# Kernel tuning notes

Hardware: AMD Instinct MI355X
Metric: run time of the kernel (lower is better)

Reference implementation:

```python
import jax, jax.numpy as jnp
import numpy as np


def setup_inputs() -> dict:
    key = jax.random.key(0)
    ks = jax.random.split(key, 6)
    B, T, D, H = 2, 2048, 1024, 16
    dk = D // H
    s = 0.02
    return {
        "x": jax.random.normal(ks[0], (B, T, D), dtype=jnp.float32),
        "Wq": jax.random.normal(ks[1], (H, dk, dk), dtype=jnp.float32) * s,
        "Wk": jax.random.normal(ks[2], (H, dk, dk), dtype=jnp.float32) * s,
        "Wv": jax.random.normal(ks[3], (H, dk, dk), dtype=jnp.float32) * s,
        "Wp": jax.random.normal(ks[4], (D, D), dtype=jnp.float32) * s,
        "bp": jnp.zeros((D,), dtype=jnp.float32),
    }


def reference(x, Wq, Wk, Wv, Wp, bp):
    B, T, D = x.shape
    H, dk, _ = Wq.shape
    # split into heads: [B, H, T, dk]
    xh = x.reshape(B, T, H, dk).transpose(0, 2, 1, 3)
    # per-head torch Linear (y = x @ W^T), all heads at once
    q = jnp.einsum('bhtd,hkd->bhtk', xh, Wq)
    k = jnp.einsum('bhtd,hkd->bhtk', xh, Wk)
    v = jnp.einsum('bhtd,hkd->bhtk', xh, Wv)
    scale = 1.0 / jnp.sqrt(jnp.float32(dk))  # original divides by sqrt(C) with C == d_k
    scores = jnp.einsum('bhqd,bhkd->bhqk', q, k) * scale
    causal = jnp.tril(jnp.ones((T, T), dtype=bool))
    scores = jnp.where(causal[None, None], scores, -jnp.inf)
    attn = jax.nn.softmax(scores, axis=-1)
    out = jnp.einsum('bhqk,bhkd->bhqd', attn, v)  # [B,H,T,dk]
    out = out.transpose(0, 2, 1, 3).reshape(B, T, D)  # concat heads
    return out @ Wp.T + bp
```

## Files before the change

### kernel.cpp

```cpp
#include <hip/hip_runtime.h>
#include <math.h>

#define B_ 2
#define T_ 2048
#define D_ 1024
#define H_ 16
#define DK 64
#define BH_ (B_*H_)

typedef __attribute__((ext_vector_type(8))) short short8;
typedef __attribute__((ext_vector_type(4))) short bf16x4;
typedef __attribute__((ext_vector_type(4))) float fragC;

__device__ __forceinline__ unsigned short f2bf(float x) {
    union { float f; unsigned u; } c; c.f = x;
    unsigned r = c.u + 0x7fff + ((c.u >> 16) & 1);
    return (unsigned short)(r >> 16);
}

__device__ __forceinline__ unsigned short f2bf_trunc(float x) {
    union { float f; unsigned u; } c; c.f = x;
    return (unsigned short)(c.u >> 16);
}

__device__ __forceinline__ unsigned pack2bf(float a, float b) {
    return (unsigned)f2bf(a) | ((unsigned)f2bf(b) << 16);
}

__device__ __forceinline__ short8 packbf8(float4 a, float4 b) {
    union { short8 v; unsigned u[4]; } r;
    r.u[0] = pack2bf(a.x, a.y); r.u[1] = pack2bf(a.z, a.w);
    r.u[2] = pack2bf(b.x, b.y); r.u[3] = pack2bf(b.z, b.w);
    return r.v;
}

__device__ __forceinline__ int swz(int row, int unit) {
    return row*64 + (((unit ^ (row & 7)) << 3));
}

__device__ __forceinline__ void gload_lds16(const void* g, void* l) {
    __builtin_amdgcn_global_load_lds(
        (const __attribute__((address_space(1))) unsigned int*)g,
        (__attribute__((address_space(3))) unsigned int*)l, 16, 0, 0);
}

__global__ __launch_bounds__(256) void cvt_kernel(
    const float* __restrict__ Wp,
    const float* __restrict__ Wq, const float* __restrict__ Wk,
    const float* __restrict__ Wv,
    unsigned short* __restrict__ Wb, unsigned short* __restrict__ wqkvb)
{
    const int gid = blockIdx.x * 256 + threadIdx.x;
    const float* src; unsigned short* dst;
    if (gid < 131072) { src = Wp + (size_t)gid * 8; dst = Wb + (size_t)gid * 8; }
    else              { int e = gid - 131072;
                        int mat = e >> 13, rem = e & 8191;
                        int h = rem >> 9, od = rem & 511;
                        const float* ws = (mat == 0) ? Wq : (mat == 1) ? Wk : Wv;
                        src = ws + ((size_t)(h << 9) + od) * 8;
                        dst = wqkvb + ((size_t)h*1536 + mat*512 + od) * 8; }
    float4 a = *(const float4*)src;
    float4 b = *(const float4*)(src + 4);
    *(uint4*)dst = make_uint4(pack2bf(a.x, a.y), pack2bf(a.z, a.w),
                              pack2bf(b.x, b.y), pack2bf(b.z, b.w));
}

__global__ __launch_bounds__(256) void qkv_kernel(
    const float* __restrict__ x,
    const unsigned short* __restrict__ wqkvb,
    unsigned short* __restrict__ q, unsigned short* __restrict__ k,
    unsigned short* __restrict__ vt)
{
    __shared__ unsigned short Wl[3*64*64];

    const int bh = blockIdx.x;
    const int b  = bh >> 4, h = bh & 15;
    const int t0 = blockIdx.y * 128;
    const int tid = threadIdx.x;
    const int wave = tid >> 6, lane = tid & 63;
    const int n = lane & 15, quad = lane >> 4;

    {
        const unsigned short* wsrc = wqkvb + (size_t)h * 12288;
        #pragma unroll
        for (int j = 0; j < 6; ++j) {
            const int off = (wave*6 + j) * 512 + lane*8;
            gload_lds16(wsrc + off, &Wl[off]);
        }
    }

    const int tw = t0 + wave*32;
    short8 xf[2][2];
    #pragma unroll
    for (int rt = 0; rt < 2; ++rt) {
        const float* xr = &x[((size_t)b*T_ + tw + rt*16 + n)*D_ + h*DK];
        float4 a0 = *(const float4*)&xr[quad*8];
        float4 a1 = *(const float4*)&xr[quad*8 + 4];
        xf[rt][0] = packbf8(a0, a1);
        float4 b0 = *(const float4*)&xr[32 + quad*8];
        float4 b1 = *(const float4*)&xr[32 + quad*8 + 4];
        xf[rt][1] = packbf8(b0, b1);
    }
    __syncthreads();

    const int tb0 = blockIdx.y*8 + wave*2;
    #pragma unroll
    for (int mat = 0; mat < 3; ++mat) {
        const int wbase = mat * 4096;
        #pragma unroll
        for (int ct = 0; ct < 4; ++ct) {
            short8 wf0 = *(const short8*)&Wl[wbase + (ct*16 + n)*64 + quad*8];
            short8 wf1 = *(const short8*)&Wl[wbase + (ct*16 + n)*64 + 32 + quad*8];
            #pragma unroll
            for (int rt = 0; rt < 2; ++rt) {
                fragC z = {0.f,0.f,0.f,0.f};
                if (mat < 2) {
                    z = __builtin_amdgcn_mfma_f32_16x16x32_bf16(wf0, xf[rt][0], z, 0,0,0);
                    z = __builtin_amdgcn_mfma_f32_16x16x32_bf16(wf1, xf[rt][1], z, 0,0,0);
                    unsigned short* dstg = (mat == 0) ? q : k;
                    unsigned short* dp = &dstg[((size_t)bh*128 + tb0 + rt)*1024
                                               + (ct*2 + (quad>>1))*128 + n*8 + (quad&1)*4];
                    *(uint2*)dp = make_uint2(pack2bf(z[0], z[1]), pack2bf(z[2], z[3]));
                } else {
                    z = __builtin_amdgcn_mfma_f32_16x16x32_bf16(xf[rt][0], wf0, z, 0,0,0);
                    z = __builtin_amdgcn_mfma_f32_16x16x32_bf16(xf[rt][1], wf1, z, 0,0,0);
                    unsigned short* dp = &vt[((size_t)bh*DK + ct*16 + n)*T_
                                             + tw + rt*16 + quad*4];
                    *(uint2*)dp = make_uint2(pack2bf(z[0], z[1]), pack2bf(z[2], z[3]));
                }
            }
        }
    }
}

__global__ __launch_bounds__(256, 4) void attn_kernel(
    const unsigned short* __restrict__ q, const unsigned short* __restrict__ k,
    const unsigned short* __restrict__ vt, unsigned short* __restrict__ aout)
{
    __shared__ unsigned short Ks[64*64];
    __shared__ unsigned short Vs[64*64];
    __shared__ unsigned short Ps[4][16][68];

    const int id = blockIdx.x;
    int qt, bh;
    if (id < 512) { bh = id >> 4;         qt = 31 - (id & 15); }
    else          { bh = (id - 512) >> 4; qt = (id - 512) & 15; }

    const int b   = bh >> 4, h = bh & 15;
    const int tid = threadIdx.x;
    const int wave = tid >> 6, lane = tid & 63;
    const int n = lane & 15, quad = lane >> 4;

    const int q0 = qt*64 + wave*16;

    const unsigned short* qb = &q[((size_t)bh*128 + qt*4 + wave)*1024 + n*8];
    short8 qf0 = *(const short8*)&qb[quad*128];
    short8 qf1 = *(const short8*)&qb[(4 + quad)*128];

    fragC o[4];
    #pragma unroll
    for (int dt = 0; dt < 4; ++dt) o[dt] = (fragC){0.f,0.f,0.f,0.f};
    fragC l4 = {0.f,0.f,0.f,0.f};

    short8 ones;
    #pragma unroll
    for (int j = 0; j < 8; ++j) ones[j] = (short)0x3F80;

    const int srow = tid >> 2;
    const int u0   = (tid & 3) * 2;
    const unsigned short* kg = &k[(size_t)bh*131072
                                  + (srow >> 4)*1024 + u0*128 + (srow & 15)*8];
    const unsigned short* vg = &vt[((size_t)bh*DK + srow)*T_ + u0*8];
    const int kl0 = swz(srow, u0), kl1 = swz(srow, u0+1);

    const int nt = qt + 1;
    short8 pk0 = *(const short8*)&kg[0], pk1 = *(const short8*)&kg[128];
    short8 pv0 = *(const short8*)&vg[0], pv1 = *(const short8*)&vg[8];

    const float sc = 0.125f * 1.44269504088896340736f;

    for (int kt = 0; kt < nt; ++kt) {
        __syncthreads();
        *(short8*)&Ks[kl0] = pk0; *(short8*)&Ks[kl1] = pk1;
        *(short8*)&Vs[kl0] = pv0; *(short8*)&Vs[kl1] = pv1;
        __syncthreads();
        if (kt + 1 < nt) {
            pk0 = *(const short8*)&kg[(size_t)(kt+1)*4096];
            pk1 = *(const short8*)&kg[(size_t)(kt+1)*4096 + 128];
            pv0 = *(const short8*)&vg[(kt+1)*64];
            pv1 = *(const short8*)&vg[(kt+1)*64 + 8];
        }
        const bool diag = (kt == qt);

        #pragma unroll
        for (int ct = 0; ct < 4; ++ct) {
            const int row = ct*16 + n;
            short8 kf0 = *(const short8*)&Ks[swz(row, quad)];
            short8 kf1 = *(const short8*)&Ks[swz(row, 4 + quad)];
            fragC c = {0.f,0.f,0.f,0.f};
            c = __builtin_amdgcn_mfma_f32_16x16x32_bf16(kf0, qf0, c, 0,0,0);
            c = __builtin_amdgcn_mfma_f32_16x16x32_bf16(kf1, qf1, c, 0,0,0);
            float p[4];
            #pragma unroll
            for (int r = 0; r < 4; ++r) p[r] = exp2f(c[r] * sc);
            if (diag) {
                const int lim = (wave*16 + n) - (ct*16 + quad*4);
                #pragma unroll
                for (int r = 0; r < 4; ++r) if (r > lim) p[r] = 0.f;
            }
            union { uint2 u; unsigned short s[4]; } w;
            w.s[0] = f2bf_trunc(p[0]); w.s[1] = f2bf_trunc(p[1]);
            w.s[2] = f2bf_trunc(p[2]); w.s[3] = f2bf_trunc(p[3]);
            *(uint2*)&Ps[wave][n][ct*16 + quad*4] = w.u;
        }
        bf16x4 a0 = *(const bf16x4*)&Ps[wave][n][quad*8];
        bf16x4 a1 = *(const bf16x4*)&Ps[wave][n][quad*8 + 4];
        bf16x4 a2 = *(const bf16x4*)&Ps[wave][n][32 + quad*8];
        bf16x4 a3 = *(const bf16x4*)&Ps[wave][n][32 + quad*8 + 4];
        short8 pf0 = __builtin_shufflevector(a0, a1, 0,1,2,3,4,5,6,7);
        short8 pf1 = __builtin_shufflevector(a2, a3, 0,1,2,3,4,5,6,7);
        l4 = __builtin_amdgcn_mfma_f32_16x16x32_bf16(ones, pf0, l4, 0,0,0);
        l4 = __builtin_amdgcn_mfma_f32_16x16x32_bf16(ones, pf1, l4, 0,0,0);
        #pragma unroll
        for (int dt = 0; dt < 4; ++dt) {
            const int row = dt*16 + n;
            short8 vf0 = *(const short8*)&Vs[swz(row, quad)];
            short8 vf1 = *(const short8*)&Vs[swz(row, 4 + quad)];
            o[dt] = __builtin_amdgcn_mfma_f32_16x16x32_bf16(vf0, pf0, o[dt], 0,0,0);
            o[dt] = __builtin_amdgcn_mfma_f32_16x16x32_bf16(vf1, pf1, o[dt], 0,0,0);
        }
    }

    const float inv = 1.0f / l4[0];
    unsigned short* dp = &aout[((size_t)b*T_ + q0 + n)*D_ + h*DK + quad*4];
    #pragma unroll
    for (int dt = 0; dt < 4; ++dt) {
        *(uint2*)(dp + dt*16) =
            make_uint2(pack2bf(o[dt][0]*inv, o[dt][1]*inv),
                       pack2bf(o[dt][2]*inv, o[dt][3]*inv));
    }
}

__global__ __launch_bounds__(256) void proj_kernel(
    const unsigned short* __restrict__ A, const unsigned short* __restrict__ Wb,
    const float* __restrict__ bp, float* __restrict__ out)
{
    __shared__ unsigned short As[128*64];
    __shared__ unsigned short Bs[128*64];

    const int m0 = blockIdx.x * 128, n0 = blockIdx.y * 128;
    const int tid = threadIdx.x;
    const int wave = tid >> 6, lane = tid & 63;
    const int wm = wave & 1, wn = wave >> 1;
    const int n = lane & 15, quad = lane >> 4;

    const int srow = wave*32 + (lane >> 3);
    const int scol = (lane & 7) * 8;
    const unsigned short* ag = &A [(size_t)(m0 + srow)*1024 + scol];
    const unsigned short* bg = &Wb[(size_t)(n0 + srow)*1024 + scol];
    unsigned short* al = &As[(size_t)srow*64 + scol];
    unsigned short* bl = &Bs[(size_t)srow*64 + scol];

    fragC acc[4][4];
    #pragma unroll
    for (int i = 0; i < 4; ++i)
        #pragma unroll
        for (int j = 0; j < 4; ++j) acc[i][j] = (fragC){0.f,0.f,0.f,0.f};

    for (int kt = 0; kt < 16; ++kt) {
        __syncthreads();
        #pragma unroll
        for (int i = 0; i < 4; ++i) {
            gload_lds16(ag + (size_t)i*8*1024 + kt*64, al + i*8*64);
            gload_lds16(bg + (size_t)i*8*1024 + kt*64, bl + i*8*64);
        }
        __syncthreads();

        #pragma unroll
        for (int kk = 0; kk < 2; ++kk) {
            short8 af[4], bf[4];
            #pragma unroll
            for (int i = 0; i < 4; ++i)
                af[i] = *(const short8*)&As[(wm*64 + i*16 + n)*64 + kk*32 + quad*8];
            #pragma unroll
            for (int j = 0; j < 4; ++j)
                bf[j] = *(const short8*)&Bs[(wn*64 + j*16 + n)*64 + kk*32 + quad*8];
            #pragma unroll
            for (int i = 0; i < 4; ++i)
                #pragma unroll
                for (int j = 0; j < 4; ++j)
                    acc[i][j] = __builtin_amdgcn_mfma_f32_16x16x32_bf16(af[i], bf[j], acc[i][j], 0,0,0);
        }
    }

    #pragma unroll
    for (int i = 0; i < 4; ++i) {
        #pragma unroll
        for (int r = 0; r < 4; ++r) {
            const int m = m0 + wm*64 + i*16 + quad*4 + r;
            #pragma unroll
            for (int j = 0; j < 4; ++j) {
                const int col = n0 + wn*64 + j*16 + n;
                out[(size_t)m*1024 + col] = acc[i][j][r] + bp[col];
            }
        }
    }
}

extern "C" void kernel_launch(void* const* d_in, const int* in_sizes, int n_in,
                              void* d_out, int out_size, void* d_ws, size_t ws_size,
                              hipStream_t stream)
{
    const float* x  = (const float*)d_in[0];
    const float* Wq = (const float*)d_in[1];
    const float* Wk = (const float*)d_in[2];
    const float* Wv = (const float*)d_in[3];
    const float* Wp = (const float*)d_in[4];
    const float* bp = (const float*)d_in[5];
    float* out = (float*)d_out;

    const size_t per = (size_t)BH_ * T_ * DK;
    unsigned short* qws   = (unsigned short*)d_ws;
    unsigned short* kws   = qws + per;
    unsigned short* vtws  = kws + per;
    unsigned short* aws   = vtws + per;
    unsigned short* wbws  = aws + per;
    unsigned short* wqkvb = wbws + 1024*1024;

    cvt_kernel<<<dim3(608), 256, 0, stream>>>(Wp, Wq, Wk, Wv, wbws, wqkvb);
    qkv_kernel<<<dim3(BH_, T_/128), 256, 0, stream>>>(x, wqkvb, qws, kws, vtws);
    attn_kernel<<<dim3(1024), 256, 0, stream>>>(qws, kws, vtws, aws);
    proj_kernel<<<dim3(32, 8), 256, 0, stream>>>(aws, wbws, bp, out);
}
```

Baseline: 153.6 us.

## Keep P in registers and double-buffer K/V via direct LDS loads

The QKV kernel now folds the softmax scale into Q and writes V in a tiled layout that matches the MFMA 16x16x16 operand order. The attention kernel drops the per-wave P staging through shared memory. It feeds the P fragments straight from registers into 16x16x16 bf16 MFMAs, packing them with a byte-permute truncation. K and V tiles are loaded with global_load_lds into double-buffered shared memory, which removes the register round-trip and one barrier per iteration. The cost is more MFMA instructions of a smaller shape, plus unswizzled LDS reads that may cause bank conflicts.

```diff
diff --git a/kernel.cpp b/kernel.cpp
--- a/kernel.cpp
+++ b/kernel.cpp
@@ -12,19 +12,26 @@
 typedef __attribute__((ext_vector_type(4))) short bf16x4;
 typedef __attribute__((ext_vector_type(4))) float fragC;
 
+#if defined(__HIP_DEVICE_COMPILE__)
+#define MFMA16(A,B,C) __builtin_amdgcn_mfma_f32_16x16x16bf16_1k((A),(B),(C),0,0,0)
+#else
+#define MFMA16(A,B,C) (C)
+#endif
+#define MFMA32(A,B,C) __builtin_amdgcn_mfma_f32_16x16x32_bf16((A),(B),(C),0,0,0)
+
 __device__ __forceinline__ unsigned short f2bf(float x) {
     union { float f; unsigned u; } c; c.f = x;
     unsigned r = c.u + 0x7fff + ((c.u >> 16) & 1);
     return (unsigned short)(r >> 16);
 }
 
-__device__ __forceinline__ unsigned short f2bf_trunc(float x) {
-    union { float f; unsigned u; } c; c.f = x;
-    return (unsigned short)(c.u >> 16);
-}
-
 __device__ __forceinline__ unsigned pack2bf(float a, float b) {
     return (unsigned)f2bf(a) | ((unsigned)f2bf(b) << 16);
+}
+
+__device__ __forceinline__ unsigned permpack(float a, float b) {
+    union { float f; unsigned u; } ca, cb; ca.f = a; cb.f = b;
+    return __builtin_amdgcn_perm(cb.u, ca.u, 0x07060302);
 }
 
 __device__ __forceinline__ short8 packbf8(float4 a, float4 b) {
@@ -32,10 +39,6 @@
     r.u[0] = pack2bf(a.x, a.y); r.u[1] = pack2bf(a.z, a.w);
     r.u[2] = pack2bf(b.x, b.y); r.u[3] = pack2bf(b.z, b.w);
     return r.v;
-}
-
-__device__ __forceinline__ int swz(int row, int unit) {
-    return row*64 + (((unit ^ (row & 7)) << 3));
 }
 
 __device__ __forceinline__ void gload_lds16(const void* g, void* l) {
@@ -103,6 +106,7 @@
     }
     __syncthreads();
 
+    const float qsc = 0.125f * 1.44269504088896340736f;
     const int tb0 = blockIdx.y*8 + wave*2;
     #pragma unroll
     for (int mat = 0; mat < 3; ++mat) {
@@ -115,17 +119,22 @@
             for (int rt = 0; rt < 2; ++rt) {
                 fragC z = {0.f,0.f,0.f,0.f};
                 if (mat < 2) {
-                    z = __builtin_amdgcn_mfma_f32_16x16x32_bf16(wf0, xf[rt][0], z, 0,0,0);
-                    z = __builtin_amdgcn_mfma_f32_16x16x32_bf16(wf1, xf[rt][1], z, 0,0,0);
+                    z = MFMA32(wf0, xf[rt][0], z);
+                    z = MFMA32(wf1, xf[rt][1], z);
+                    if (mat == 0) {
+                        z[0] *= qsc; z[1] *= qsc; z[2] *= qsc; z[3] *= qsc;
+                    }
                     unsigned short* dstg = (mat == 0) ? q : k;
                     unsigned short* dp = &dstg[((size_t)bh*128 + tb0 + rt)*1024
                                                + (ct*2 + (quad>>1))*128 + n*8 + (quad&1)*4];
                     *(uint2*)dp = make_uint2(pack2bf(z[0], z[1]), pack2bf(z[2], z[3]));
                 } else {
-                    z = __builtin_amdgcn_mfma_f32_16x16x32_bf16(xf[rt][0], wf0, z, 0,0,0);
-                    z = __builtin_amdgcn_mfma_f32_16x16x32_bf16(xf[rt][1], wf1, z, 0,0,0);
-                    unsigned short* dp = &vt[((size_t)bh*DK + ct*16 + n)*T_
-                                             + tw + rt*16 + quad*4];
+                    z = MFMA32(xf[rt][0], wf0, z);
+                    z = MFMA32(xf[rt][1], wf1, z);
+                    const int key0 = tw + rt*16;
+                    const int ktv = key0 >> 6, ctv = (key0 >> 4) & 3;
+                    unsigned short* dp = &vt[(size_t)bh*131072 + ktv*4096
+                                             + ct*1024 + ctv*256 + quad*64 + n*4];
                     *(uint2*)dp = make_uint2(pack2bf(z[0], z[1]), pack2bf(z[2], z[3]));
                 }
             }
@@ -137,9 +146,8 @@
     const unsigned short* __restrict__ q, const unsigned short* __restrict__ k,
     const unsigned short* __restrict__ vt, unsigned short* __restrict__ aout)
 {
-    __shared__ unsigned short Ks[64*64];
-    __shared__ unsigned short Vs[64*64];
-    __shared__ unsigned short Ps[4][16][68];
+    __shared__ unsigned short Ks[2][4096];
+    __shared__ unsigned short Vs[2][4096];
 
     const int id = blockIdx.x;
     int qt, bh;
@@ -150,7 +158,6 @@
     const int tid = threadIdx.x;
     const int wave = tid >> 6, lane = tid & 63;
     const int n = lane & 15, quad = lane >> 4;
-
     const int q0 = qt*64 + wave*16;
 
     const unsigned short* qb = &q[((size_t)bh*128 + qt*4 + wave)*1024 + n*8];
@@ -162,72 +169,66 @@
     for (int dt = 0; dt < 4; ++dt) o[dt] = (fragC){0.f,0.f,0.f,0.f};
     fragC l4 = {0.f,0.f,0.f,0.f};
 
-    short8 ones;
-    #pragma unroll
-    for (int j = 0; j < 8; ++j) ones[j] = (short)0x3F80;
-
-    const int srow = tid >> 2;
-    const int u0   = (tid & 3) * 2;
-    const unsigned short* kg = &k[(size_t)bh*131072
-                                  + (srow >> 4)*1024 + u0*128 + (srow & 15)*8];
-    const unsigned short* vg = &vt[((size_t)bh*DK + srow)*T_ + u0*8];
-    const int kl0 = swz(srow, u0), kl1 = swz(srow, u0+1);
+    bf16x4 ones4;
+    #pragma unroll
+    for (int j = 0; j < 4; ++j) ones4[j] = (short)0x3F80;
+
+    const unsigned short* kg = &k[(size_t)bh*131072];
+    const unsigned short* vg = &vt[(size_t)bh*131072];
 
     const int nt = qt + 1;
-    short8 pk0 = *(const short8*)&kg[0], pk1 = *(const short8*)&kg[128];
-    short8 pv0 = *(const short8*)&vg[0], pv1 = *(const short8*)&vg[8];
-
-    const float sc = 0.125f * 1.44269504088896340736f;
+    gload_lds16(kg + tid*8,        &Ks[0][tid*8]);
+    gload_lds16(kg + 2048 + tid*8, &Ks[0][2048 + tid*8]);
+    gload_lds16(vg + tid*8,        &Vs[0][tid*8]);
+    gload_lds16(vg + 2048 + tid*8, &Vs[0][2048 + tid*8]);
 
     for (int kt = 0; kt < nt; ++kt) {
         __syncthreads();
-        *(short8*)&Ks[kl0] = pk0; *(short8*)&Ks[kl1] = pk1;
-        *(short8*)&Vs[kl0] = pv0; *(short8*)&Vs[kl1] = pv1;
-        __syncthreads();
         if (kt + 1 < nt) {
-            pk0 = *(const short8*)&kg[(size_t)(kt+1)*4096];
-            pk1 = *(const short8*)&kg[(size_t)(kt+1)*4096 + 128];
-            pv0 = *(const short8*)&vg[(kt+1)*64];
-            pv1 = *(const short8*)&vg[(kt+1)*64 + 8];
-        }
+            const int nb = (kt + 1) & 1;
+            const unsigned short* kgn = kg + (size_t)(kt+1)*4096;
+            const unsigned short* vgn = vg + (size_t)(kt+1)*4096;
+            gload_lds16(kgn + tid*8,        &Ks[nb][tid*8]);
+            gload_lds16(kgn + 2048 + tid*8, &Ks[nb][2048 + tid*8]);
+            gload_lds16(vgn + tid*8,        &Vs[nb][tid*8]);
+            gload_lds16(vgn + 2048 + tid*8, &Vs[nb][2048 + tid*8]);
+        }
+        const unsigned short* Kb = Ks[kt & 1];
+        const unsigned short* Vb = Vs[kt & 1];
         const bool diag = (kt == qt);
 
+        bf16x4 pp[4];
         #pragma unroll
         for (int ct = 0; ct < 4; ++ct) {
-            const int row = ct*16 + n;
-            short8 kf0 = *(const short8*)&Ks[swz(row, quad)];
-            short8 kf1 = *(const short8*)&Ks[swz(row, 4 + quad)];
+            short8 kf0 = *(const short8*)&Kb[ct*1024 + quad*128 + n*8];
+            short8 kf1 = *(const short8*)&Kb[ct*1024 + 512 + quad*128 + n*8];
             fragC c = {0.f,0.f,0.f,0.f};
-            c = __builtin_amdgcn_mfma_f32_16x16x32_bf16(kf0, qf0, c, 0,0,0);
-            c = __builtin_amdgcn_mfma_f32_16x16x32_bf16(kf1, qf1, c, 0,0,0);
-            float p[4];
-            #pragma unroll
-            for (int r = 0; r < 4; ++r) p[r] = exp2f(c[r] * sc);
+            c = MFMA32(kf0, qf0, c);
+            c = MFMA32(kf1, qf1, c);
+            float p0 = exp2f(c[0]), p1 = exp2f(c[1]);
+            float p2 = exp2f(c[2]), p3 = exp2f(c[3]);
             if (diag) {
                 const int lim = (wave*16 + n) - (ct*16 + quad*4);
-                #pragma unroll
-                for (int r = 0; r < 4; ++r) if (r > lim) p[r] = 0.f;
+                if (0 > lim) p0 = 0.f;
+                if (1 > lim) p1 = 0.f;
+                if (2 > lim) p2 = 0.f;
+                if (3 > lim) p3 = 0.f;
             }
-            union { uint2 u; unsigned short s[4]; } w;
-            w.s[0] = f2bf_trunc(p[0]); w.s[1] = f2bf_trunc(p[1]);
-            w.s[2] = f2bf_trunc(p[2]); w.s[3] = f2bf_trunc(p[3]);
-            *(uint2*)&Ps[wave][n][ct*16 + quad*4] = w.u;
-        }
-        bf16x4 a0 = *(const bf16x4*)&Ps[wave][n][quad*8];
-        bf16x4 a1 = *(const bf16x4*)&Ps[wave][n][quad*8 + 4];
-        bf16x4 a2 = *(const bf16x4*)&Ps[wave][n][32 + quad*8];
-        bf16x4 a3 = *(const bf16x4*)&Ps[wave][n][32 + quad*8 + 4];
-        short8 pf0 = __builtin_shufflevector(a0, a1, 0,1,2,3,4,5,6,7);
-        short8 pf1 = __builtin_shufflevector(a2, a3, 0,1,2,3,4,5,6,7);
-        l4 = __builtin_amdgcn_mfma_f32_16x16x32_bf16(ones, pf0, l4, 0,0,0);
-        l4 = __builtin_amdgcn_mfma_f32_16x16x32_bf16(ones, pf1, l4, 0,0,0);
+            union { bf16x4 v; unsigned u[2]; } pk;
+            pk.u[0] = permpack(p0, p1);
+            pk.u[1] = permpack(p2, p3);
+            pp[ct] = pk.v;
+        }
+        #pragma unroll
+        for (int ct = 0; ct < 4; ++ct)
+            l4 = MFMA16(ones4, pp[ct], l4);
         #pragma unroll
         for (int dt = 0; dt < 4; ++dt) {
-            const int row = dt*16 + n;
-            short8 vf0 = *(const short8*)&Vs[swz(row, quad)];
-            short8 vf1 = *(const short8*)&Vs[swz(row, 4 + quad)];
-            o[dt] = __builtin_amdgcn_mfma_f32_16x16x32_bf16(vf0, pf0, o[dt], 0,0,0);
-            o[dt] = __builtin_amdgcn_mfma_f32_16x16x32_bf16(vf1, pf1, o[dt], 0,0,0);
+            #pragma unroll
+            for (int ct = 0; ct < 4; ++ct) {
+                bf16x4 vf = *(const bf16x4*)&Vb[dt*1024 + ct*256 + quad*64 + n*4];
+                o[dt] = MFMA16(vf, pp[ct], o[dt]);
+            }
         }
     }
 
@@ -289,7 +290,7 @@
             for (int i = 0; i < 4; ++i)
                 #pragma unroll
                 for (int j = 0; j < 4; ++j)
-                    acc[i][j] = __builtin_amdgcn_mfma_f32_16x16x32_bf16(af[i], bf[j], acc[i][j], 0,0,0);
+                    acc[i][j] = MFMA32(af[i], bf[j], acc[i][j]);
         }
     }
 
```

Result: faster. 149.3 us (-2.8%).
